# Kernel tuning notes

Measured on AMD Instinct MI355X. Metric: run time of the kernel, lower is better.

Reference implementation:

```python
import jax, jax.numpy as jnp
import numpy as np

N = 100000
E = 1600000
F_IN, H, C = 128, 128, 64


def setup_inputs() -> dict:
    key = jax.random.key(0)
    ks = jax.random.split(key, 8)
    x = jax.random.normal(ks[0], (N, F_IN), dtype=jnp.float32)
    edge_index = jax.random.randint(ks[1], (2, E), 0, N, dtype=jnp.int64)
    s = lambda fi: (1.0 / np.sqrt(fi))
    # SAGEConv1: lin_l (applied to mean-aggregated neighbors, has bias), lin_r (root, no bias)
    W1l = jax.random.uniform(ks[2], (H, F_IN), jnp.float32, -s(F_IN), s(F_IN))
    b1 = jnp.zeros((H,), jnp.float32)
    W1r = jax.random.uniform(ks[3], (H, F_IN), jnp.float32, -s(F_IN), s(F_IN))
    # SAGEConv2
    W2l = jax.random.uniform(ks[4], (C, H), jnp.float32, -s(H), s(H))
    b2 = jnp.zeros((C,), jnp.float32)
    W2r = jax.random.uniform(ks[5], (C, H), jnp.float32, -s(H), s(H))
    return {"x": x, "edge_index": edge_index, "W1l": W1l, "b1": b1, "W1r": W1r,
            "W2l": W2l, "b2": b2, "W2r": W2r}


def _mean_aggr(x, src, dst):
    # mean over incoming neighbors (PyG flow: edge_index[0]=source -> edge_index[1]=target)
    msg = x[src]                                            # [E, F] big gather
    summed = jax.ops.segment_sum(msg, dst, num_segments=N)  # [N, F]
    cnt = jax.ops.segment_sum(jnp.ones((src.shape[0],), x.dtype), dst, num_segments=N)
    return summed / jnp.clip(cnt, 1.0)[:, None]


def _sage_conv(x, src, dst, Wl, b, Wr):
    agg = _mean_aggr(x, src, dst)
    return agg @ Wl.T + b + x @ Wr.T


def _iconv(x, src, dst):
    # weight-free GCN propagation: D^-1/2 (A + I) D^-1/2 @ x
    loops = jnp.arange(N, dtype=src.dtype)
    s2 = jnp.concatenate([src, loops])
    d2 = jnp.concatenate([dst, loops])
    deg = jax.ops.segment_sum(jnp.ones((s2.shape[0],), x.dtype), d2, num_segments=N)
    dis = jnp.where(deg > 0, jax.lax.rsqrt(jnp.maximum(deg, 1.0)), 0.0)
    norm = dis[s2] * dis[d2]                               # [E+N]
    return jax.ops.segment_sum(norm[:, None] * x[s2], d2, num_segments=N)


def reference(x, edge_index, W1l, b1, W1r, W2l, b2, W2r):
    src, dst = edge_index[0], edge_index[1]
    h = jax.nn.relu(_sage_conv(x, src, dst, W1l, b1, W1r))
    # F.dropout(training=False) -> identity in eval mode
    h = _sage_conv(h, src, dst, W2l, b2, W2r)
    return _iconv(h, src, dst)
```

## Files before the change

### kernel.cpp

```cpp
#include <hip/hip_runtime.h>

#define GN 100000
#define GE 1600000
#define GF 128
#define GH 128
#define GC 64

#define NB 392
#define SLABSZ 5376
#define P1_EDGES 4096
#define P1_BLOCKS ((GE + P1_EDGES - 1) / P1_EDGES)
#define CASTX_BLOCKS 12500

typedef __attribute__((ext_vector_type(8))) short v8s;
typedef __attribute__((ext_vector_type(4))) float v4f;

__device__ __forceinline__ unsigned short f2bf(float f) {
    union { float f; unsigned u; } a; a.f = f;
    unsigned r = a.u + 0x7fff + ((a.u >> 16) & 1);
    return (unsigned short)(r >> 16);
}
__device__ __forceinline__ float bf2f(unsigned short b) {
    union { unsigned u; float f; } a; a.u = ((unsigned)b) << 16;
    return a.f;
}

__global__ __launch_bounds__(256) void prep_kernel(
    unsigned* __restrict__ slab, int* __restrict__ bucket_cnt,
    const int* __restrict__ src, const int* __restrict__ dst,
    unsigned short* __restrict__ xb, const float* __restrict__ x,
    unsigned short* w1l, unsigned short* w1r,
    unsigned short* w2l, unsigned short* w2r,
    const float* W1l, const float* W1r,
    const float* W2l, const float* W2r)
{
    __shared__ int hist[512];
    __shared__ int scanex[512];
    __shared__ int cursor[512];
    __shared__ int gbase[512];
    __shared__ int ssum[256];
    __shared__ unsigned stage[P1_EDGES];
    __shared__ unsigned short sbid[P1_EDGES];

    int tid = threadIdx.x;
    int blk = blockIdx.x;

    if (blk >= P1_BLOCKS) {
        int cb = blk - P1_BLOCKS;
        if (cb < CASTX_BLOCKS) {
            int i = cb * 256 + tid;
            float4 v = ((const float4*)x)[i];
            ushort4 u;
            u.x = f2bf(v.x); u.y = f2bf(v.y); u.z = f2bf(v.z); u.w = f2bf(v.w);
            ((ushort4*)xb)[i] = u;
            return;
        }
        int i = (cb - CASTX_BLOCKS) * 256 + tid;
        const float* s; unsigned short* d; int off;
        if      (i <  4096) { s = W1l; d = w1l; off = i; }
        else if (i <  8192) { s = W1r; d = w1r; off = i - 4096; }
        else if (i < 10240) { s = W2l; d = w2l; off = i - 8192; }
        else if (i < 12288) { s = W2r; d = w2r; off = i - 10240; }
        else return;
        float4 v = ((const float4*)s)[off];
        ushort4 u;
        u.x = f2bf(v.x); u.y = f2bf(v.y); u.z = f2bf(v.z); u.w = f2bf(v.w);
        ((ushort4*)d)[off] = u;
        return;
    }

    int e0 = blk * P1_EDGES;
    int nE = min(P1_EDGES, GE - e0);

    unsigned pk[16]; int bk[16];
    hist[tid] = 0; hist[tid + 256] = 0;
    __syncthreads();
    #pragma unroll
    for (int j = 0; j < 16; ++j) {
        int i = j * 256 + tid;
        if (i < nE) {
            int e = e0 + i;
            int d = dst[e], s = src[e];
            int b = d >> 8;
            pk[j] = ((unsigned)(d & 255) << 17) | (unsigned)s;
            bk[j] = b;
            atomicAdd(&hist[b], 1);
        } else bk[j] = -1;
    }
    __syncthreads();
    int a0 = hist[2 * tid], a1 = hist[2 * tid + 1];
    int s2 = a0 + a1;
    ssum[tid] = s2;
    __syncthreads();
    for (int off = 1; off < 256; off <<= 1) {
        int v = (tid >= off) ? ssum[tid - off] : 0;
        __syncthreads();
        ssum[tid] += v;
        __syncthreads();
    }
    int pbase = ssum[tid] - s2;
    scanex[2 * tid] = pbase;          cursor[2 * tid] = pbase;
    scanex[2 * tid + 1] = pbase + a0; cursor[2 * tid + 1] = pbase + a0;
    __syncthreads();
    #pragma unroll
    for (int j = 0; j < 16; ++j) {
        if (bk[j] >= 0) {
            int pos = atomicAdd(&cursor[bk[j]], 1);
            stage[pos] = pk[j];
            sbid[pos] = (unsigned short)bk[j];
        }
    }
    for (int b = tid; b < NB; b += 256) {
        int c = hist[b];
        gbase[b] = c ? atomicAdd(&bucket_cnt[b], c) : 0;
    }
    __syncthreads();
    for (int i = tid; i < nE; i += 256) {
        int b = sbid[i];
        int go = gbase[b] + (i - scanex[b]);
        if (go < SLABSZ)
            slab[(size_t)b * SLABSZ + go] = stage[i];
    }
}

__global__ __launch_bounds__(256) void bucket_pass2_kernel(
    int* __restrict__ csr, int* __restrict__ row_ptr,
    float* __restrict__ invc, float* __restrict__ dis,
    const unsigned* __restrict__ slab, const int* __restrict__ bucket_cnt)
{
    __shared__ int deg_l[256];
    __shared__ int excl[256];
    __shared__ int cur[256];
    __shared__ int ssum[256];
    __shared__ int bstart_s;
    __shared__ unsigned stage[SLABSZ];

    int t = threadIdx.x;
    int b = blockIdx.x;

    int c0 = (2 * t < NB) ? bucket_cnt[2 * t] : 0;
    int c1 = (2 * t + 1 < NB) ? bucket_cnt[2 * t + 1] : 0;
    int sc = c0 + c1;
    ssum[t] = sc;
    __syncthreads();
    for (int off = 1; off < 256; off <<= 1) {
        int v = (t >= off) ? ssum[t - off] : 0;
        __syncthreads();
        ssum[t] += v;
        __syncthreads();
    }
    int pb = ssum[t] - sc;
    if (2 * t == b)     bstart_s = pb;
    if (2 * t + 1 == b) bstart_s = pb + c0;
    if (b == NB - 1 && t == 0) row_ptr[GN] = GE;

    int cnt = min(bucket_cnt[b], SLABSZ);
    const unsigned* sp = slab + (size_t)b * SLABSZ;
    deg_l[t] = 0;
    __syncthreads();
    int base = bstart_s;
    for (int i = t; i < cnt; i += 256)
        atomicAdd(&deg_l[sp[i] >> 17], 1);
    __syncthreads();
    int dg = deg_l[t];
    ssum[t] = dg;
    __syncthreads();
    for (int off = 1; off < 256; off <<= 1) {
        int v = (t >= off) ? ssum[t - off] : 0;
        __syncthreads();
        ssum[t] += v;
        __syncthreads();
    }
    int ex = ssum[t] - dg;
    excl[t] = ex; cur[t] = ex;
    __syncthreads();
    int d = b * 256 + t;
    if (d < GN) {
        row_ptr[d] = base + ex;
        float c = (float)dg;
        invc[d] = 1.0f / fmaxf(c, 1.0f);
        dis[d] = rsqrtf(c + 1.0f);
    }
    for (int i = t; i < cnt; i += 256) {
        unsigned p = sp[i];
        int pos = atomicAdd(&cur[p >> 17], 1);
        stage[pos] = p & 0x1FFFFu;
    }
    __syncthreads();
    for (int i = t; i < cnt; i += 256)
        csr[base + i] = (int)stage[i];
}

__global__ __launch_bounds__(64, 2) void fused_gemm_kernel(
    unsigned short* __restrict__ P, unsigned short* __restrict__ Q,
    const unsigned short* __restrict__ A1, const unsigned short* __restrict__ A2,
    const unsigned short* __restrict__ W1, const unsigned short* __restrict__ W2,
    const unsigned short* __restrict__ Wl, const unsigned short* __restrict__ Wr,
    const float* __restrict__ b1, const float* __restrict__ b2, int M)
{
    __shared__ unsigned short hs[64][136];

    int lane = threadIdx.x;
    int lm = lane & 15, quad = lane >> 4;
    int m_base = blockIdx.x * 64;

    v4f acc[4][8];
    #pragma unroll
    for (int mt = 0; mt < 4; ++mt)
        #pragma unroll
        for (int nt = 0; nt < 8; ++nt) acc[mt][nt] = (v4f){0.f,0.f,0.f,0.f};

    #pragma unroll
    for (int ks = 0; ks < 4; ++ks) {
        int koff = ks * 32 + quad * 8;
        v8s a1[4], a2[4];
        #pragma unroll
        for (int mt = 0; mt < 4; ++mt) {
            int row = m_base + mt * 16 + lm;
            if (row < M) {
                a1[mt] = *(const v8s*)(A1 + (size_t)row * 128 + koff);
                a2[mt] = *(const v8s*)(A2 + (size_t)row * 128 + koff);
            } else {
                a1[mt] = (v8s){0,0,0,0,0,0,0,0};
                a2[mt] = (v8s){0,0,0,0,0,0,0,0};
            }
        }
        v8s w1[8], w2[8];
        #pragma unroll
        for (int nt = 0; nt < 8; ++nt) {
            int col = nt * 16 + lm;
            w1[nt] = *(const v8s*)(W1 + (size_t)col * 128 + koff);
            w2[nt] = *(const v8s*)(W2 + (size_t)col * 128 + koff);
        }
        #pragma unroll
        for (int mt = 0; mt < 4; ++mt)
            #pragma unroll
            for (int nt = 0; nt < 8; ++nt) {
                acc[mt][nt] = __builtin_amdgcn_mfma_f32_16x16x32_bf16(a1[mt], w1[nt], acc[mt][nt], 0, 0, 0);
                acc[mt][nt] = __builtin_amdgcn_mfma_f32_16x16x32_bf16(a2[mt], w2[nt], acc[mt][nt], 0, 0, 0);
            }
    }

    #pragma unroll
    for (int mt = 0; mt < 4; ++mt)
        #pragma unroll
        for (int r = 0; r < 4; ++r) {
            int rl = mt * 16 + quad * 4 + r;
            #pragma unroll
            for (int nt = 0; nt < 8; ++nt) {
                int col = nt * 16 + lm;
                float v = acc[mt][nt][r] + b1[col];
                hs[rl][col] = f2bf(fmaxf(v, 0.f));
            }
        }

    v4f accP[4][4], accQ[4][4];
    #pragma unroll
    for (int mt = 0; mt < 4; ++mt)
        #pragma unroll
        for (int nt = 0; nt < 4; ++nt) {
            accP[mt][nt] = (v4f){0.f,0.f,0.f,0.f};
            accQ[mt][nt] = (v4f){0.f,0.f,0.f,0.f};
        }

    #pragma unroll
    for (int ks = 0; ks < 4; ++ks) {
        int koff = ks * 32 + quad * 8;
        v8s af[4], bl[4], br[4];
        #pragma unroll
        for (int mt = 0; mt < 4; ++mt)
            af[mt] = *(const v8s*)&hs[mt * 16 + lm][koff];
        #pragma unroll
        for (int nt = 0; nt < 4; ++nt) {
            int col = nt * 16 + lm;
            bl[nt] = *(const v8s*)(Wl + (size_t)col * 128 + koff);
            br[nt] = *(const v8s*)(Wr + (size_t)col * 128 + koff);
        }
        #pragma unroll
        for (int mt = 0; mt < 4; ++mt)
            #pragma unroll
            for (int nt = 0; nt < 4; ++nt) {
                accP[mt][nt] = __builtin_amdgcn_mfma_f32_16x16x32_bf16(af[mt], bl[nt], accP[mt][nt], 0, 0, 0);
                accQ[mt][nt] = __builtin_amdgcn_mfma_f32_16x16x32_bf16(af[mt], br[nt], accQ[mt][nt], 0, 0, 0);
            }
    }

    #pragma unroll
    for (int mt = 0; mt < 4; ++mt)
        #pragma unroll
        for (int r = 0; r < 4; ++r) {
            int row = m_base + mt * 16 + quad * 4 + r;
            if (row >= M) continue;
            #pragma unroll
            for (int nt = 0; nt < 4; ++nt) {
                int col = nt * 16 + lm;
                P[(size_t)row * 64 + col] = f2bf(accP[mt][nt][r]);
                Q[(size_t)row * 64 + col] = f2bf(accQ[mt][nt][r] + b2[col]);
            }
        }
}

__global__ __launch_bounds__(256) void gather_mean128_kernel(
    unsigned short* __restrict__ out, const unsigned short* __restrict__ in,
    const float* __restrict__ invc, const int* __restrict__ row_ptr,
    const int* __restrict__ csr, int N)
{
    int wid = (blockIdx.x * 256 + threadIdx.x) >> 6;
    int lane = threadIdx.x & 63;
    if (wid >= N) return;
    int beg = __builtin_amdgcn_readfirstlane(row_ptr[wid]);
    int end = __builtin_amdgcn_readfirstlane(row_ptr[wid + 1]);
    int d = end - beg;
    float a0 = 0.f, a1 = 0.f;
    if (d > 0) {
        int dc = min(d, 64);
        int idx = csr[beg + ((lane < dc) ? lane : (dc - 1))];
        for (int t = 0; t < dc; t += 16) {
            unsigned v[16];
            #pragma unroll
            for (int u = 0; u < 16; ++u) {
                int tt = t + u;
                int s = __builtin_amdgcn_readlane(idx, (tt < dc) ? tt : (dc - 1));
                unsigned x = ((const unsigned*)(in + (size_t)s * 128))[lane];
                v[u] = (tt < dc) ? x : 0u;
            }
            #pragma unroll
            for (int u = 0; u < 16; ++u) {
                a0 += bf2f((unsigned short)(v[u] & 0xffff));
                a1 += bf2f((unsigned short)(v[u] >> 16));
            }
        }
        for (int j = beg + 64; j < end; ++j) {
            int s = __builtin_amdgcn_readfirstlane(csr[j]);
            unsigned x = ((const unsigned*)(in + (size_t)s * 128))[lane];
            a0 += bf2f((unsigned short)(x & 0xffff));
            a1 += bf2f((unsigned short)(x >> 16));
        }
    }
    float ic = invc[wid];
    unsigned o = (unsigned)f2bf(a0 * ic) | ((unsigned)f2bf(a1 * ic) << 16);
    ((unsigned*)(out + (size_t)wid * 128))[lane] = o;
}

__global__ __launch_bounds__(256) void gather_combine_kernel(
    unsigned short* __restrict__ h2s, const unsigned short* __restrict__ p,
    const unsigned short* __restrict__ q,
    const float* __restrict__ invc, const float* __restrict__ dis,
    const int* __restrict__ row_ptr, const int* __restrict__ csr, int N)
{
    int wid = (blockIdx.x * 256 + threadIdx.x) >> 6;
    int lane = threadIdx.x & 63;
    if (wid >= N) return;
    int beg = __builtin_amdgcn_readfirstlane(row_ptr[wid]);
    int end = __builtin_amdgcn_readfirstlane(row_ptr[wid + 1]);
    int d = end - beg;
    float a = 0.f;
    if (d > 0) {
        int dc = min(d, 64);
        int idx = csr[beg + ((lane < dc) ? lane : (dc - 1))];
        for (int t = 0; t < dc; t += 16) {
            unsigned short v[16];
            #pragma unroll
            for (int u = 0; u < 16; ++u) {
                int tt = t + u;
                int s = __builtin_amdgcn_readlane(idx, (tt < dc) ? tt : (dc - 1));
                unsigned short x = p[(size_t)s * 64 + lane];
                v[u] = (tt < dc) ? x : (unsigned short)0;
            }
            #pragma unroll
            for (int u = 0; u < 16; ++u) a += bf2f(v[u]);
        }
        for (int j = beg + 64; j < end; ++j) {
            int s = __builtin_amdgcn_readfirstlane(csr[j]);
            a += bf2f(p[(size_t)s * 64 + lane]);
        }
    }
    float ic = invc[wid], dd = dis[wid];
    float qv = bf2f(q[(size_t)wid * 64 + lane]);
    h2s[(size_t)wid * 64 + lane] = f2bf(dd * (a * ic + qv));
}

__global__ __launch_bounds__(256) void iconv_kernel(
    float* __restrict__ out, const unsigned short* __restrict__ h2s,
    const float* __restrict__ dis, const int* __restrict__ row_ptr,
    const int* __restrict__ csr, int N)
{
    int wid = (blockIdx.x * 256 + threadIdx.x) >> 6;
    int lane = threadIdx.x & 63;
    if (wid >= N) return;
    int beg = __builtin_amdgcn_readfirstlane(row_ptr[wid]);
    int end = __builtin_amdgcn_readfirstlane(row_ptr[wid + 1]);
    int d = end - beg;
    float a = 0.f;
    if (d > 0) {
        int dc = min(d, 64);
        int idx = csr[beg + ((lane < dc) ? lane : (dc - 1))];
        for (int t = 0; t < dc; t += 16) {
            unsigned short v[16];
            #pragma unroll
            for (int u = 0; u < 16; ++u) {
                int tt = t + u;
                int s = __builtin_amdgcn_readlane(idx, (tt < dc) ? tt : (dc - 1));
                unsigned short x = h2s[(size_t)s * 64 + lane];
                v[u] = (tt < dc) ? x : (unsigned short)0;
            }
            #pragma unroll
            for (int u = 0; u < 16; ++u) a += bf2f(v[u]);
        }
        for (int j = beg + 64; j < end; ++j) {
            int s = __builtin_amdgcn_readfirstlane(csr[j]);
            a += bf2f(h2s[(size_t)s * 64 + lane]);
        }
    }
    a += bf2f(h2s[(size_t)wid * 64 + lane]);
    out[(size_t)wid * 64 + lane] = dis[wid] * a;
}

extern "C" void kernel_launch(void* const* d_in, const int* in_sizes, int n_in,
                              void* d_out, int out_size, void* d_ws, size_t ws_size,
                              hipStream_t stream) {
    const float* x   = (const float*)d_in[0];
    const int*   ei  = (const int*)d_in[1];
    const float* W1l = (const float*)d_in[2];
    const float* b1  = (const float*)d_in[3];
    const float* W1r = (const float*)d_in[4];
    const float* W2l = (const float*)d_in[5];
    const float* b2  = (const float*)d_in[6];
    const float* W2r = (const float*)d_in[7];
    float* out = (float*)d_out;

    const int* src = ei;
    const int* dst = ei + GE;

    float* invc = (float*)d_ws;
    float* dis  = invc + GN;
    unsigned short* regA = (unsigned short*)(dis + GN);
    unsigned short* regB = regA + (size_t)GN * 128;
    unsigned short* xb    = regA;
    unsigned short* aggx  = regB;
    unsigned short* w1lb = regB + (size_t)GN * 128;
    unsigned short* w1rb = w1lb + GH * GF;
    unsigned short* w2lb = w1rb + GH * GF;
    unsigned short* w2rb = w2lb + GC * GH;
    int* row_ptr      = (int*)(w2rb + GC * GH);
    int* bucket_cnt   = row_ptr + GN + 1;
    unsigned* slab    = (unsigned*)(bucket_cnt + NB);
    int* csr          = (int*)(slab + (size_t)NB * SLABSZ);
    unsigned short* pq = (unsigned short*)(csr + GE);
    unsigned short* pb = pq;
    unsigned short* qb = pq + (size_t)GN * 64;
    unsigned short* h2s = regB;

    const int T = 256;
    const int g_wave = (GN * 64 + T - 1) / T;
    dim3 g_fused((GN + 63) / 64, 1);

    hipMemsetAsync(bucket_cnt, 0, NB * sizeof(int), stream);
    prep_kernel<<<P1_BLOCKS + CASTX_BLOCKS + 48, T, 0, stream>>>(
        slab, bucket_cnt, src, dst,
        xb, x, w1lb, w1rb, w2lb, w2rb, W1l, W1r, W2l, W2r);

    bucket_pass2_kernel<<<NB, T, 0, stream>>>(csr, row_ptr, invc, dis,
                                              slab, bucket_cnt);

    gather_mean128_kernel<<<g_wave, T, 0, stream>>>(aggx, xb, invc, row_ptr, csr, GN);

    fused_gemm_kernel<<<g_fused, 64, 0, stream>>>(pb, qb, aggx, xb,
                                                  w1lb, w1rb, w2lb, w2rb,
                                                  b1, b2, GN);

    gather_combine_kernel<<<g_wave, T, 0, stream>>>(h2s, pb, qb, invc, dis,
                                                    row_ptr, csr, GN);

    iconv_kernel<<<g_wave, T, 0, stream>>>(out, h2s, dis, row_ptr, csr, GN);
}
```

Baseline: 339.7 us.

## Gather multiple neighbor rows per wavefront with 16-byte vector loads and shuffle reduction

The three CSR gather kernels now split each wavefront into lane groups that each fetch a different neighbor row with uint4 (16-byte) loads, 4 rows at a time for the 128-wide features and 8 for the 64-wide ones. Partial sums are combined across groups with xor shuffles and only the first group writes the output. This replaces per-lane 2- or 4-byte loads, one row per step, with wider loads that keep more rows in flight. In exchange it adds shuffle reductions and partly idle lanes in the tail step and the final store.

```diff
diff --git a/kernel.cpp b/kernel.cpp
--- a/kernel.cpp
+++ b/kernel.cpp
@@ -14,6 +14,7 @@
 
 typedef __attribute__((ext_vector_type(8))) short v8s;
 typedef __attribute__((ext_vector_type(4))) float v4f;
+typedef __attribute__((ext_vector_type(2))) float v2f;
 
 __device__ __forceinline__ unsigned short f2bf(float f) {
     union { float f; unsigned u; } a; a.f = f;
@@ -23,6 +24,11 @@
 __device__ __forceinline__ float bf2f(unsigned short b) {
     union { unsigned u; float f; } a; a.u = ((unsigned)b) << 16;
     return a.f;
+}
+__device__ __forceinline__ v2f cvt2(unsigned w) {
+    union { unsigned u; float f; } lo, hi;
+    lo.u = w << 16; hi.u = w & 0xffff0000u;
+    return (v2f){lo.f, hi.f};
 }
 
 __global__ __launch_bounds__(256) void prep_kernel(
@@ -311,35 +317,52 @@
     int beg = __builtin_amdgcn_readfirstlane(row_ptr[wid]);
     int end = __builtin_amdgcn_readfirstlane(row_ptr[wid + 1]);
     int d = end - beg;
-    float a0 = 0.f, a1 = 0.f;
-    if (d > 0) {
-        int dc = min(d, 64);
-        int idx = csr[beg + ((lane < dc) ? lane : (dc - 1))];
-        for (int t = 0; t < dc; t += 16) {
-            unsigned v[16];
-            #pragma unroll
-            for (int u = 0; u < 16; ++u) {
-                int tt = t + u;
-                int s = __builtin_amdgcn_readlane(idx, (tt < dc) ? tt : (dc - 1));
-                unsigned x = ((const unsigned*)(in + (size_t)s * 128))[lane];
-                v[u] = (tt < dc) ? x : 0u;
-            }
-            #pragma unroll
-            for (int u = 0; u < 16; ++u) {
-                a0 += bf2f((unsigned short)(v[u] & 0xffff));
-                a1 += bf2f((unsigned short)(v[u] >> 16));
-            }
-        }
-        for (int j = beg + 64; j < end; ++j) {
-            int s = __builtin_amdgcn_readfirstlane(csr[j]);
-            unsigned x = ((const unsigned*)(in + (size_t)s * 128))[lane];
-            a0 += bf2f((unsigned short)(x & 0xffff));
-            a1 += bf2f((unsigned short)(x >> 16));
-        }
-    }
-    float ic = invc[wid];
-    unsigned o = (unsigned)f2bf(a0 * ic) | ((unsigned)f2bf(a1 * ic) << 16);
-    ((unsigned*)(out + (size_t)wid * 128))[lane] = o;
+    int grp = lane >> 4, lx = lane & 15;
+    v2f a0 = {0.f,0.f}, a1 = {0.f,0.f}, a2 = {0.f,0.f}, a3 = {0.f,0.f};
+
+    int nf = d >> 2;
+    #pragma unroll 4
+    for (int t = 0; t < nf; ++t) {
+        int j = beg + t * 4;
+        int s0 = csr[j], s1 = csr[j + 1], s2 = csr[j + 2], s3 = csr[j + 3];
+        int sa = (lane & 16) ? s1 : s0;
+        int sb = (lane & 16) ? s3 : s2;
+        int ss = (lane & 32) ? sb : sa;
+        uint4 v = ((const uint4*)(in + (size_t)ss * 128))[lx];
+        a0 += cvt2(v.x); a1 += cvt2(v.y); a2 += cvt2(v.z); a3 += cvt2(v.w);
+    }
+    int rem = d & 3;
+    if (rem) {
+        int j = beg + nf * 4;
+        int c1 = (rem > 1) ? 1 : 0;
+        int c2 = (rem > 2) ? 2 : c1;
+        int s0 = csr[j], s1 = csr[j + c1], s2 = csr[j + c2], s3 = s2;
+        int sa = (lane & 16) ? s1 : s0;
+        int sb = (lane & 16) ? s3 : s2;
+        int ss = (lane & 32) ? sb : sa;
+        uint4 v = ((const uint4*)(in + (size_t)ss * 128))[lx];
+        bool ok = grp < rem;
+        v.x = ok ? v.x : 0u; v.y = ok ? v.y : 0u;
+        v.z = ok ? v.z : 0u; v.w = ok ? v.w : 0u;
+        a0 += cvt2(v.x); a1 += cvt2(v.y); a2 += cvt2(v.z); a3 += cvt2(v.w);
+    }
+    a0.x += __shfl_xor(a0.x, 16); a0.y += __shfl_xor(a0.y, 16);
+    a1.x += __shfl_xor(a1.x, 16); a1.y += __shfl_xor(a1.y, 16);
+    a2.x += __shfl_xor(a2.x, 16); a2.y += __shfl_xor(a2.y, 16);
+    a3.x += __shfl_xor(a3.x, 16); a3.y += __shfl_xor(a3.y, 16);
+    a0.x += __shfl_xor(a0.x, 32); a0.y += __shfl_xor(a0.y, 32);
+    a1.x += __shfl_xor(a1.x, 32); a1.y += __shfl_xor(a1.y, 32);
+    a2.x += __shfl_xor(a2.x, 32); a2.y += __shfl_xor(a2.y, 32);
+    a3.x += __shfl_xor(a3.x, 32); a3.y += __shfl_xor(a3.y, 32);
+    if (grp == 0) {
+        float ic = invc[wid];
+        uint4 o;
+        o.x = (unsigned)f2bf(a0.x * ic) | ((unsigned)f2bf(a0.y * ic) << 16);
+        o.y = (unsigned)f2bf(a1.x * ic) | ((unsigned)f2bf(a1.y * ic) << 16);
+        o.z = (unsigned)f2bf(a2.x * ic) | ((unsigned)f2bf(a2.y * ic) << 16);
+        o.w = (unsigned)f2bf(a3.x * ic) | ((unsigned)f2bf(a3.y * ic) << 16);
+        ((uint4*)(out + (size_t)wid * 128))[lx] = o;
+    }
 }
 
 __global__ __launch_bounds__(256) void gather_combine_kernel(
@@ -354,30 +377,59 @@
     int beg = __builtin_amdgcn_readfirstlane(row_ptr[wid]);
     int end = __builtin_amdgcn_readfirstlane(row_ptr[wid + 1]);
     int d = end - beg;
-    float a = 0.f;
-    if (d > 0) {
-        int dc = min(d, 64);
-        int idx = csr[beg + ((lane < dc) ? lane : (dc - 1))];
-        for (int t = 0; t < dc; t += 16) {
-            unsigned short v[16];
-            #pragma unroll
-            for (int u = 0; u < 16; ++u) {
-                int tt = t + u;
-                int s = __builtin_amdgcn_readlane(idx, (tt < dc) ? tt : (dc - 1));
-                unsigned short x = p[(size_t)s * 64 + lane];
-                v[u] = (tt < dc) ? x : (unsigned short)0;
-            }
-            #pragma unroll
-            for (int u = 0; u < 16; ++u) a += bf2f(v[u]);
-        }
-        for (int j = beg + 64; j < end; ++j) {
-            int s = __builtin_amdgcn_readfirstlane(csr[j]);
-            a += bf2f(p[(size_t)s * 64 + lane]);
-        }
-    }
-    float ic = invc[wid], dd = dis[wid];
-    float qv = bf2f(q[(size_t)wid * 64 + lane]);
-    h2s[(size_t)wid * 64 + lane] = f2bf(dd * (a * ic + qv));
+    int grp = lane >> 3, lx = lane & 7;
+    v2f a0 = {0.f,0.f}, a1 = {0.f,0.f}, a2 = {0.f,0.f}, a3 = {0.f,0.f};
+
+    int nf = d >> 3;
+    #pragma unroll 2
+    for (int t = 0; t < nf; ++t) {
+        int j = beg + t * 8;
+        int s0 = csr[j],     s1 = csr[j + 1], s2 = csr[j + 2], s3 = csr[j + 3];
+        int s4 = csr[j + 4], s5 = csr[j + 5], s6 = csr[j + 6], s7 = csr[j + 7];
+        int t0 = (lane & 8) ? s1 : s0; int t1 = (lane & 8) ? s3 : s2;
+        int t2 = (lane & 8) ? s5 : s4; int t3 = (lane & 8) ? s7 : s6;
+        int u0 = (lane & 16) ? t1 : t0; int u1 = (lane & 16) ? t3 : t2;
+        int ss = (lane & 32) ? u1 : u0;
+        uint4 v = ((const uint4*)(p + (size_t)ss * 64))[lx];
+        a0 += cvt2(v.x); a1 += cvt2(v.y); a2 += cvt2(v.z); a3 += cvt2(v.w);
+    }
+    int rem = d & 7;
+    if (rem) {
+        int j = beg + nf * 8;
+        int rc = rem - 1;
+        int s0 = csr[j];
+        int s1 = csr[j + min(1, rc)]; int s2 = csr[j + min(2, rc)];
+        int s3 = csr[j + min(3, rc)]; int s4 = csr[j + min(4, rc)];
+        int s5 = csr[j + min(5, rc)]; int s6 = csr[j + min(6, rc)];
+        int s7 = csr[j + min(7, rc)];
+        int t0 = (lane & 8) ? s1 : s0; int t1 = (lane & 8) ? s3 : s2;
+        int t2 = (lane & 8) ? s5 : s4; int t3 = (lane & 8) ? s7 : s6;
+        int u0 = (lane & 16) ? t1 : t0; int u1 = (lane & 16) ? t3 : t2;
+        int ss = (lane & 32) ? u1 : u0;
+        uint4 v = ((const uint4*)(p + (size_t)ss * 64))[lx];
+        bool ok = grp < rem;
+        v.x = ok ? v.x : 0u; v.y = ok ? v.y : 0u;
+        v.z = ok ? v.z : 0u; v.w = ok ? v.w : 0u;
+        a0 += cvt2(v.x); a1 += cvt2(v.y); a2 += cvt2(v.z); a3 += cvt2(v.w);
+    }
+    #pragma unroll
+    for (int m = 8; m <= 32; m <<= 1) {
+        a0.x += __shfl_xor(a0.x, m); a0.y += __shfl_xor(a0.y, m);
+        a1.x += __shfl_xor(a1.x, m); a1.y += __shfl_xor(a1.y, m);
+        a2.x += __shfl_xor(a2.x, m); a2.y += __shfl_xor(a2.y, m);
+        a3.x += __shfl_xor(a3.x, m); a3.y += __shfl_xor(a3.y, m);
+    }
+    if (grp == 0) {
+        float ic = invc[wid], dd = dis[wid];
+        uint4 qv = ((const uint4*)(q + (size_t)wid * 64))[lx];
+        v2f q0 = cvt2(qv.x), q1 = cvt2(qv.y), q2 = cvt2(qv.z), q3 = cvt2(qv.w);
+        uint4 o;
+        o.x = (unsigned)f2bf(dd * (a0.x * ic + q0.x)) | ((unsigned)f2bf(dd * (a0.y * ic + q0.y)) << 16);
+        o.y = (unsigned)f2bf(dd * (a1.x * ic + q1.x)) | ((unsigned)f2bf(dd * (a1.y * ic + q1.y)) << 16);
+        o.z = (unsigned)f2bf(dd * (a2.x * ic + q2.x)) | ((unsigned)f2bf(dd * (a2.y * ic + q2.y)) << 16);
+        o.w = (unsigned)f2bf(dd * (a3.x * ic + q3.x)) | ((unsigned)f2bf(dd * (a3.y * ic + q3.y)) << 16);
+        ((uint4*)(h2s + (size_t)wid * 64))[lx] = o;
+    }
 }
 
 __global__ __launch_bounds__(256) void iconv_kernel(
@@ -391,29 +443,59 @@
     int beg = __builtin_amdgcn_readfirstlane(row_ptr[wid]);
     int end = __builtin_amdgcn_readfirstlane(row_ptr[wid + 1]);
     int d = end - beg;
-    float a = 0.f;
-    if (d > 0) {
-        int dc = min(d, 64);
-        int idx = csr[beg + ((lane < dc) ? lane : (dc - 1))];
-        for (int t = 0; t < dc; t += 16) {
-            unsigned short v[16];
-            #pragma unroll
-            for (int u = 0; u < 16; ++u) {
-                int tt = t + u;
-                int s = __builtin_amdgcn_readlane(idx, (tt < dc) ? tt : (dc - 1));
-                unsigned short x = h2s[(size_t)s * 64 + lane];
-                v[u] = (tt < dc) ? x : (unsigned short)0;
-            }
-            #pragma unroll
-            for (int u = 0; u < 16; ++u) a += bf2f(v[u]);
-        }
-        for (int j = beg + 64; j < end; ++j) {
-            int s = __builtin_amdgcn_readfirstlane(csr[j]);
-            a += bf2f(h2s[(size_t)s * 64 + lane]);
-        }
-    }
-    a += bf2f(h2s[(size_t)wid * 64 + lane]);
-    out[(size_t)wid * 64 + lane] = dis[wid] * a;
+    int grp = lane >> 3, lx = lane & 7;
+    v2f a0 = {0.f,0.f}, a1 = {0.f,0.f}, a2 = {0.f,0.f}, a3 = {0.f,0.f};
+
+    int nf = d >> 3;
+    #pragma unroll 2
+    for (int t = 0; t < nf; ++t) {
+        int j = beg + t * 8;
+        int s0 = csr[j],     s1 = csr[j + 1], s2 = csr[j + 2], s3 = csr[j + 3];
+        int s4 = csr[j + 4], s5 = csr[j + 5], s6 = csr[j + 6], s7 = csr[j + 7];
+        int t0 = (lane & 8) ? s1 : s0; int t1 = (lane & 8) ? s3 : s2;
+        int t2 = (lane & 8) ? s5 : s4; int t3 = (lane & 8) ? s7 : s6;
+        int u0 = (lane & 16) ? t1 : t0; int u1 = (lane & 16) ? t3 : t2;
+        int ss = (lane & 32) ? u1 : u0;
+        uint4 v = ((const uint4*)(h2s + (size_t)ss * 64))[lx];
+        a0 += cvt2(v.x); a1 += cvt2(v.y); a2 += cvt2(v.z); a3 += cvt2(v.w);
+    }
+    int rem = d & 7;
+    if (rem) {
+        int j = beg + nf * 8;
+        int rc = rem - 1;
+        int s0 = csr[j];
+        int s1 = csr[j + min(1, rc)]; int s2 = csr[j + min(2, rc)];
+        int s3 = csr[j + min(3, rc)]; int s4 = csr[j + min(4, rc)];
+        int s5 = csr[j + min(5, rc)]; int s6 = csr[j + min(6, rc)];
+        int s7 = csr[j + min(7, rc)];
+        int t0 = (lane & 8) ? s1 : s0; int t1 = (lane & 8) ? s3 : s2;
+        int t2 = (lane & 8) ? s5 : s4; int t3 = (lane & 8) ? s7 : s6;
+        int u0 = (lane & 16) ? t1 : t0; int u1 = (lane & 16) ? t3 : t2;
+        int ss = (lane & 32) ? u1 : u0;
+        uint4 v = ((const uint4*)(h2s + (size_t)ss * 64))[lx];
+        bool ok = grp < rem;
+        v.x = ok ? v.x : 0u; v.y = ok ? v.y : 0u;
+        v.z = ok ? v.z : 0u; v.w = ok ? v.w : 0u;
+        a0 += cvt2(v.x); a1 += cvt2(v.y); a2 += cvt2(v.z); a3 += cvt2(v.w);
+    }
+    #pragma unroll
+    for (int m = 8; m <= 32; m <<= 1) {
+        a0.x += __shfl_xor(a0.x, m); a0.y += __shfl_xor(a0.y, m);
+        a1.x += __shfl_xor(a1.x, m); a1.y += __shfl_xor(a1.y, m);
+        a2.x += __shfl_xor(a2.x, m); a2.y += __shfl_xor(a2.y, m);
+        a3.x += __shfl_xor(a3.x, m); a3.y += __shfl_xor(a3.y, m);
+    }
+    if (grp == 0) {
+        uint4 sv = ((const uint4*)(h2s + (size_t)wid * 64))[lx];
+        v2f s0 = cvt2(sv.x), s1 = cvt2(sv.y), s2 = cvt2(sv.z), s3 = cvt2(sv.w);
+        float dd = dis[wid];
+        float4 o0 = make_float4(dd * (a0.x + s0.x), dd * (a0.y + s0.y),
+                                dd * (a1.x + s1.x), dd * (a1.y + s1.y));
+        float4 o1 = make_float4(dd * (a2.x + s2.x), dd * (a2.y + s2.y),
+                                dd * (a3.x + s3.x), dd * (a3.y + s3.y));
+        ((float4*)(out + (size_t)wid * 64))[lx * 2]     = o0;
+        ((float4*)(out + (size_t)wid * 64))[lx * 2 + 1] = o1;
+    }
 }
 
 extern "C" void kernel_launch(void* const* d_in, const int* in_sizes, int n_in,
```

New measurement: 335.2 us. No clear change (-1.3%).
